# Kernel optimization log

Hardware: AMD Instinct MI355X
Metric: run time of the kernel (lower is better)

Reference implementation:

```python
import jax, jax.numpy as jnp
import numpy as np

H = 16
D_MODEL = 1024
HEAD_DIM = D_MODEL // H
NEG = -1e9


def setup_inputs() -> dict:
    key = jax.random.key(0)
    k1, k2, k3, k4, k5, k6 = jax.random.split(key, 6)
    B, L = 2, 2048
    feature = jax.random.normal(k1, (B, L, D_MODEL), dtype=jnp.float32)
    mask = jax.random.randint(k2, (B, L), 0, 2, dtype=jnp.int32)
    # Linear weights stored torch-style as [out, in]; biases zero-init per initialize().
    s = 1.0 / np.sqrt(D_MODEL)
    W_Q = jax.random.uniform(k3, (D_MODEL, D_MODEL), jnp.float32, -s, s)
    W_K = jax.random.uniform(k4, (D_MODEL, D_MODEL), jnp.float32, -s, s)
    W_V = jax.random.uniform(k5, (D_MODEL, D_MODEL), jnp.float32, -s, s)
    b_Q = jnp.zeros((D_MODEL,), jnp.float32)
    b_K = jnp.zeros((D_MODEL,), jnp.float32)
    b_V = jnp.zeros((D_MODEL,), jnp.float32)
    return {"feature": feature, "mask": mask, "W_Q": W_Q, "b_Q": b_Q,
            "W_K": W_K, "b_K": b_K, "W_V": W_V, "b_V": b_V}


def reference(feature, mask, W_Q, b_Q, W_K, b_K, W_V, b_V):
    B, L, _ = feature.shape
    scale = jnp.sqrt(jnp.float32(HEAD_DIM))
    # Projections: torch Linear is x @ W^T + b. Split into heads: [B, H, L, Dh]
    def proj(W, b):
        y = feature @ W.T + b
        return y.reshape(B, L, H, HEAD_DIM).transpose(0, 2, 1, 3)
    Q = proj(W_Q, b_Q)
    K = proj(W_K, b_K)
    V = proj(W_V, b_V)
    # Scores [B, H, Lq, Lk]
    A = jnp.einsum('bhqd,bhkd->bhqk', Q, K) / scale
    # Key-side mask broadcast over heads and query positions
    A = jnp.where(mask[:, None, None, :] == 0, jnp.float32(NEG), A)
    alpha = jax.nn.softmax(A, axis=-1)
    out = jnp.einsum('bhqk,bhkd->bhqd', alpha, V)  # [B, H, L, Dh]
    return out.transpose(0, 2, 1, 3).reshape(B, L, H * HEAD_DIM)
```

## Files before the change

### kernel.cpp

```cpp
#include <hip/hip_runtime.h>

typedef __bf16 bf16;
typedef __attribute__((ext_vector_type(4))) __bf16 bf16x4;
typedef __attribute__((ext_vector_type(8))) __bf16 bf16x8;
typedef __attribute__((ext_vector_type(4))) float f32x4;
typedef __attribute__((ext_vector_type(16))) float f32x16;
typedef unsigned int u32;

#define D_MODEL 1024
#define SEQ_L   2048
#define NHEAD   16
#define HDIM    64
#define MROWS   4096

#define S_SCALE 0.18033688f

#define FEAT_OFF  512u
#define WQ_OFF    (FEAT_OFF + 4194304u)
#define WK_OFF    (WQ_OFF + 1048576u)
#define WV_OFF    (WK_OFF + 1048576u)
#define BQ_OFF    (WV_OFF + 1048576u)
#define BK_OFF    (BQ_OFF + 1024u)
#define BV_OFF    (BK_OFF + 1024u)
#define Q_OFF     (BV_OFF + 1024u)
#define K_OFF     (Q_OFF + 4194304u)
#define V_OFF     (K_OFF + 4194304u)

typedef const __attribute__((address_space(1))) u32* gp_t;
typedef __attribute__((address_space(3))) u32* lp_t;
__device__ __forceinline__ void ld16(const bf16* g, bf16* l) {
    __builtin_amdgcn_global_load_lds((gp_t)g, (lp_t)l, 16, 0, 0);
}

__global__ void convert_in(const float* __restrict__ feat,
                           const float* __restrict__ wq, const float* __restrict__ wk,
                           const float* __restrict__ wv,
                           const float* __restrict__ bq, const float* __restrict__ bk,
                           const float* __restrict__ bv,
                           bf16* __restrict__ ws) {
    const int bid = blockIdx.x;
    const float* src; bf16* dst; int off; float sc = 1.0f;
    if (bid < 4096)      { src = feat; dst = ws + FEAT_OFF; off = bid * 1024; }
    else if (bid < 5120) { src = wq;   dst = ws + WQ_OFF;   off = (bid - 4096) * 1024; sc = S_SCALE; }
    else if (bid < 6144) { src = wk;   dst = ws + WK_OFF;   off = (bid - 5120) * 1024; }
    else if (bid < 7168) { src = wv;   dst = ws + WV_OFF;   off = (bid - 6144) * 1024; }
    else if (bid == 7168){ src = bq;   dst = ws + BQ_OFF;   off = 0; sc = S_SCALE; }
    else if (bid == 7169){ src = bk;   dst = ws + BK_OFF;   off = 0; }
    else                 { src = bv;   dst = ws + BV_OFF;   off = 0; }
    int idx = off + threadIdx.x * 4;
    float4 v = *(const float4*)(src + idx);
    bf16x4 o;
    o[0] = (bf16)(v.x * sc);
    o[1] = (bf16)(v.y * sc);
    o[2] = (bf16)(v.z * sc);
    o[3] = (bf16)(v.w * sc);
    *(bf16x4*)(dst + idx) = o;
}

__global__ __launch_bounds__(256, 2) void qkv_gemm(const bf16* __restrict__ ws,
                                                   bf16* __restrict__ wsw,
                                                   const int* __restrict__ mask) {
    __shared__ bf16 smem[3 * 128 * 64];
    bf16* Alds = smem;
    bf16* B0   = smem + 8192;
    bf16* B1   = smem + 16384;

    const int zi   = blockIdx.z;
    const int t    = threadIdx.x;
    const int lane = t & 63;
    const int wave = t >> 6;
    const int quad = lane >> 4;
    const int l16  = lane & 15;
    const int wrow = (wave >> 1) * 64;
    const int wcol = (wave & 1) * 64;
    const int r8 = lane >> 3;
    const int sl = lane & 7;
    const int sg = sl ^ r8;

    if (zi == 0) {
        const bf16* X   = ws + FEAT_OFF;
        const bf16* Wq  = ws + WQ_OFF;
        const bf16* Wk  = ws + WK_OFF;
        const int m0 = blockIdx.x * 128;
        const int n0 = blockIdx.y * 128;

        f32x4 aq[4][4], ak[4][4];
        for (int mi = 0; mi < 4; ++mi)
            for (int ni = 0; ni < 4; ++ni) {
                aq[mi][ni] = (f32x4){0.f, 0.f, 0.f, 0.f};
                ak[mi][ni] = (f32x4){0.f, 0.f, 0.f, 0.f};
            }

        for (int k0 = 0; k0 < D_MODEL; k0 += 64) {
#pragma unroll
            for (int i = 0; i < 4; ++i) {
                int ch  = wave * 4 + i;
                int row = ch * 8 + r8;
                ld16(X  + (size_t)(m0 + row) * D_MODEL + k0 + sg * 8, Alds + ch * 512);
                ld16(Wq + (size_t)(n0 + row) * D_MODEL + k0 + sg * 8, B0   + ch * 512);
                ld16(Wk + (size_t)(n0 + row) * D_MODEL + k0 + sg * 8, B1   + ch * 512);
            }
            __syncthreads();

#pragma unroll
            for (int kk = 0; kk < 2; ++kk) {
                const int sgb = quad + kk * 4;
                bf16x8 af[4];
#pragma unroll
                for (int mi = 0; mi < 4; ++mi) {
                    int row = wrow + mi * 16 + l16;
                    af[mi] = *(const bf16x8*)(&Alds[row * 64 + ((sgb ^ (row & 7)) << 3)]);
                }
                {
                    bf16x8 bfr[4];
#pragma unroll
                    for (int ni = 0; ni < 4; ++ni) {
                        int row = wcol + ni * 16 + l16;
                        bfr[ni] = *(const bf16x8*)(&B0[row * 64 + ((sgb ^ (row & 7)) << 3)]);
                    }
#pragma unroll
                    for (int mi = 0; mi < 4; ++mi)
#pragma unroll
                        for (int ni = 0; ni < 4; ++ni)
                            aq[mi][ni] = __builtin_amdgcn_mfma_f32_16x16x32_bf16(
                                af[mi], bfr[ni], aq[mi][ni], 0, 0, 0);
                }
                {
                    bf16x8 bfr[4];
#pragma unroll
                    for (int ni = 0; ni < 4; ++ni) {
                        int row = wcol + ni * 16 + l16;
                        bfr[ni] = *(const bf16x8*)(&B1[row * 64 + ((sgb ^ (row & 7)) << 3)]);
                    }
#pragma unroll
                    for (int mi = 0; mi < 4; ++mi)
#pragma unroll
                        for (int ni = 0; ni < 4; ++ni)
                            ak[mi][ni] = __builtin_amdgcn_mfma_f32_16x16x32_bf16(
                                af[mi], bfr[ni], ak[mi][ni], 0, 0, 0);
                }
            }
            __syncthreads();
        }

        bf16* Yq = wsw + Q_OFF;
        bf16* Yk = wsw + K_OFF;
        const bf16* bq = ws + BQ_OFF;
        const bf16* bk = ws + BK_OFF;
#pragma unroll
        for (int ni = 0; ni < 4; ++ni) {
            int col = n0 + wcol + ni * 16 + l16;
            float bqf = (float)bq[col];
            float bkf = (float)bk[col];
#pragma unroll
            for (int mi = 0; mi < 4; ++mi) {
                int rowb = m0 + wrow + mi * 16 + quad * 4;
#pragma unroll
                for (int r = 0; r < 4; ++r) {
                    Yq[(size_t)(rowb + r) * D_MODEL + col] = (bf16)(aq[mi][ni][r] + bqf);
                    float v = ak[mi][ni][r] + bkf;
                    if (mask[rowb + r] == 0) v = 0.f;
                    Yk[(size_t)(rowb + r) * D_MODEL + col] = (bf16)v;
                }
            }
        }
    } else {
        const bf16* Amat = ws + WV_OFF;
        const bf16* Bmat = ws + FEAT_OFF;
        const bf16* bias = ws + BV_OFF;
        bf16* Y = wsw + V_OFF;
        const int m0 = blockIdx.y * 128;
        const int n0 = blockIdx.x * 128;

        f32x4 acc[4][4];
        for (int mi = 0; mi < 4; ++mi)
            for (int ni = 0; ni < 4; ++ni)
                acc[mi][ni] = (f32x4){0.f, 0.f, 0.f, 0.f};

        for (int k0 = 0; k0 < D_MODEL; k0 += 64) {
#pragma unroll
            for (int i = 0; i < 4; ++i) {
                int ch  = wave * 4 + i;
                int row = ch * 8 + r8;
                ld16(Amat + (size_t)(m0 + row) * D_MODEL + k0 + sg * 8, Alds + ch * 512);
                ld16(Bmat + (size_t)(n0 + row) * D_MODEL + k0 + sg * 8, B0   + ch * 512);
            }
            __syncthreads();

#pragma unroll
            for (int kk = 0; kk < 2; ++kk) {
                const int sgb = quad + kk * 4;
                bf16x8 af[4], bfr[4];
#pragma unroll
                for (int mi = 0; mi < 4; ++mi) {
                    int row = wrow + mi * 16 + l16;
                    af[mi] = *(const bf16x8*)(&Alds[row * 64 + ((sgb ^ (row & 7)) << 3)]);
                }
#pragma unroll
                for (int ni = 0; ni < 4; ++ni) {
                    int row = wcol + ni * 16 + l16;
                    bfr[ni] = *(const bf16x8*)(&B0[row * 64 + ((sgb ^ (row & 7)) << 3)]);
                }
#pragma unroll
                for (int mi = 0; mi < 4; ++mi)
#pragma unroll
                    for (int ni = 0; ni < 4; ++ni)
                        acc[mi][ni] = __builtin_amdgcn_mfma_f32_16x16x32_bf16(
                            af[mi], bfr[ni], acc[mi][ni], 0, 0, 0);
            }
            __syncthreads();
        }

#pragma unroll
        for (int mi = 0; mi < 4; ++mi) {
#pragma unroll
            for (int r = 0; r < 4; ++r) {
                int rowv = m0 + wrow + mi * 16 + quad * 4 + r;
                float bvf = (float)bias[rowv];
#pragma unroll
                for (int ni = 0; ni < 4; ++ni) {
                    int col = n0 + wcol + ni * 16 + l16;
                    float v = acc[mi][ni][r] + bvf;
                    if (mask[col] == 0) v = 0.f;
                    size_t addr = (size_t)(col >> 11) * 2097152u +
                                  (size_t)rowv * 2048u + (col & 2047);
                    Y[addr] = (bf16)v;
                }
            }
        }
    }
}

__global__ __launch_bounds__(256, 4) void attn_kernel(
    const bf16* __restrict__ ws,
    const int* __restrict__ mask, float* __restrict__ out) {
    const int bh  = blockIdx.x;
    const int qt  = blockIdx.y;
    const int b   = bh >> 4, h = bh & 15;
    const int t    = threadIdx.x;
    const int lane = t & 63;
    const int wave = t >> 6;
    const int half = lane >> 5;
    const int l31  = lane & 31;

    __shared__ bf16 Klds[2][64 * 64];
    __shared__ bf16 Vlds[2][64 * 64];

    const bf16* Qh  = ws + Q_OFF + (size_t)(b * SEQ_L) * D_MODEL + h * HDIM;
    const bf16* Kh  = ws + K_OFF + (size_t)(b * SEQ_L) * D_MODEL + h * HDIM;
    const bf16* Vth = ws + V_OFF + (size_t)b * 2097152u + (size_t)(h * HDIM) * SEQ_L;

    const int qrow0 = qt * 128 + wave * 32;
    bf16x8 qf[4];
#pragma unroll
    for (int ks = 0; ks < 4; ++ks)
        qf[ks] = *(const bf16x8*)(Qh + (size_t)(qrow0 + l31) * D_MODEL
                                  + ks * 16 + half * 8);

    bf16x8 ones;
#pragma unroll
    for (int j = 0; j < 8; ++j) ones[j] = (bf16)1.0f;

    f32x16 o[2], lacc;
    int nm = 0;
#pragma unroll
    for (int i = 0; i < 16; ++i) { o[0][i] = 0.f; o[1][i] = 0.f; lacc[i] = 0.f; }

    const int srow = (lane >> 3);
    const int sg   = (lane & 7) ^ srow;

#define STAGE(bb, kt)                                                          \
    do {                                                                       \
        _Pragma("unroll")                                                      \
        for (int i = 0; i < 2; ++i) {                                          \
            int row = i * 32 + wave * 8 + srow;                                \
            ld16(Kh + (size_t)((kt) + row) * D_MODEL + sg * 8,                 \
                 &Klds[bb][i * 2048 + wave * 512]);                            \
            ld16(Vth + (size_t)row * SEQ_L + (kt) + sg * 8,                    \
                 &Vlds[bb][i * 2048 + wave * 512]);                            \
        }                                                                      \
    } while (0)

    STAGE(0, 0);
    __syncthreads();

    int cur = 0;
    for (int kt = 0; kt < SEQ_L; kt += 64) {
        if (kt + 64 < SEQ_L) STAGE(cur ^ 1, kt + 64);

        int mv = mask[b * SEQ_L + kt + lane];
        nm += (int)__popcll(__ballot(mv != 0));

        f32x16 st[2];
#pragma unroll
        for (int ktile = 0; ktile < 2; ++ktile) {
#pragma unroll
            for (int i = 0; i < 16; ++i) st[ktile][i] = 0.f;
#pragma unroll
            for (int ks = 0; ks < 4; ++ks) {
                const int row  = ktile * 32 + l31;
                const int slot = (ks * 2 + half) ^ (l31 & 7);
                bf16x8 kf = *(const bf16x8*)(&Klds[cur][row * 64 + slot * 8]);
                st[ktile] = __builtin_amdgcn_mfma_f32_32x32x16_bf16(
                    kf, qf[ks], st[ktile], 0, 0, 0);
            }
        }

        bf16x4 pk[2][4];
#pragma unroll
        for (int ktile = 0; ktile < 2; ++ktile) {
#pragma unroll
            for (int g = 0; g < 4; ++g) {
                bf16x4 pkv;
#pragma unroll
                for (int j = 0; j < 4; ++j)
                    pkv[j] = (bf16)__builtin_amdgcn_exp2f(st[ktile][g * 4 + j]);
                pk[ktile][g] = pkv;
            }
        }

        bf16x8 pf[4];
#pragma unroll
        for (int ks = 0; ks < 4; ++ks) {
            const int k1 = ks & 1, kt2 = ks >> 1;
            uint2 a  = __builtin_bit_cast(uint2, pk[kt2][2 * k1]);
            uint2 bb = __builtin_bit_cast(uint2, pk[kt2][2 * k1 + 1]);
            uint2 keep, send;
            keep.x = half ? bb.x : a.x;  keep.y = half ? bb.y : a.y;
            send.x = half ? a.x : bb.x;  send.y = half ? a.y : bb.y;
            uint2 recv;
            recv.x = (unsigned)__shfl_xor((int)send.x, 32);
            recv.y = (unsigned)__shfl_xor((int)send.y, 32);
            uint4 frag;
            frag.x = half ? recv.x : keep.x;
            frag.y = half ? recv.y : keep.y;
            frag.z = half ? keep.x : recv.x;
            frag.w = half ? keep.y : recv.y;
            pf[ks] = __builtin_bit_cast(bf16x8, frag);
        }

#pragma unroll
        for (int ks = 0; ks < 4; ++ks)
            lacc = __builtin_amdgcn_mfma_f32_32x32x16_bf16(pf[ks], ones, lacc, 0, 0, 0);
#pragma unroll
        for (int dt = 0; dt < 2; ++dt) {
#pragma unroll
            for (int ks = 0; ks < 4; ++ks) {
                const int row  = dt * 32 + l31;
                const int slot = (ks * 2 + half) ^ (l31 & 7);
                bf16x8 vf = *(const bf16x8*)(&Vlds[cur][row * 64 + slot * 8]);
                o[dt] = __builtin_amdgcn_mfma_f32_32x32x16_bf16(
                    pf[ks], vf, o[dt], 0, 0, 0);
            }
        }

        __syncthreads();
        cur ^= 1;
    }
#undef STAGE

    const float corr = (float)(SEQ_L - nm);
#pragma unroll
    for (int r = 0; r < 16; ++r) {
        const int q32 = (r & 3) + 8 * (r >> 2) + 4 * half;
        const int q = qrow0 + q32;
        const size_t base = ((size_t)(b * SEQ_L + q)) * D_MODEL + h * HDIM;
        const float rl = 1.0f / fmaxf(lacc[r] - corr, 1e-30f);
        out[base + l31]      = o[0][r] * rl;
        out[base + 32 + l31] = o[1][r] * rl;
    }
}

extern "C" void kernel_launch(void* const* d_in, const int* in_sizes, int n_in,
                              void* d_out, int out_size, void* d_ws, size_t ws_size,
                              hipStream_t stream) {
    const float* feat = (const float*)d_in[0];
    const int*   mask = (const int*)d_in[1];
    const float* Wq = (const float*)d_in[2];
    const float* bq = (const float*)d_in[3];
    const float* Wk = (const float*)d_in[4];
    const float* bk = (const float*)d_in[5];
    const float* Wv = (const float*)d_in[6];
    const float* bv = (const float*)d_in[7];

    bf16* ws = (bf16*)d_ws;

    convert_in<<<7171, 256, 0, stream>>>(feat, Wq, Wk, Wv, bq, bk, bv, ws);

    dim3 g1(32, 8, 2);
    qkv_gemm<<<g1, 256, 0, stream>>>(ws, ws, mask);

    dim3 g2(2 * NHEAD, SEQ_L / 128);
    attn_kernel<<<g2, 256, 0, stream>>>(ws, mask, (float*)d_out);
}
```

Before: 171.6 us.

## Split key range across two wave groups per block and merge via LDS

Doubles the attention block to 512 threads, with two groups of four waves each processing half of the key sequence for the same query rows. Partial outputs and row sums from the second group are written to shared memory and added by the first group before normalization. This is meant to raise parallelism and shorten the serial key loop per block. In exchange it doubles LDS use per block and adds a final reduction step.

```diff
diff --git a/kernel.cpp b/kernel.cpp
--- a/kernel.cpp
+++ b/kernel.cpp
@@ -231,7 +231,7 @@
     }
 }
 
-__global__ __launch_bounds__(256, 4) void attn_kernel(
+__global__ __launch_bounds__(512, 4) void attn_kernel(
     const bf16* __restrict__ ws,
     const int* __restrict__ mask, float* __restrict__ out) {
     const int bh  = blockIdx.x;
@@ -240,17 +240,21 @@
     const int t    = threadIdx.x;
     const int lane = t & 63;
     const int wave = t >> 6;
+    const int qh   = wave & 3;
+    const int kh   = wave >> 2;
     const int half = lane >> 5;
     const int l31  = lane & 31;
-
-    __shared__ bf16 Klds[2][64 * 64];
-    __shared__ bf16 Vlds[2][64 * 64];
+    const int kt0  = kh * 1024;
+
+    __shared__ bf16 smem[32768];
+    bf16* Kb = smem;
+    bf16* Vb = smem + 16384;
 
     const bf16* Qh  = ws + Q_OFF + (size_t)(b * SEQ_L) * D_MODEL + h * HDIM;
     const bf16* Kh  = ws + K_OFF + (size_t)(b * SEQ_L) * D_MODEL + h * HDIM;
     const bf16* Vth = ws + V_OFF + (size_t)b * 2097152u + (size_t)(h * HDIM) * SEQ_L;
 
-    const int qrow0 = qt * 128 + wave * 32;
+    const int qrow0 = qt * 128 + qh * 32;
     bf16x8 qf[4];
 #pragma unroll
     for (int ks = 0; ks < 4; ++ks)
@@ -273,24 +277,26 @@
     do {                                                                       \
         _Pragma("unroll")                                                      \
         for (int i = 0; i < 2; ++i) {                                          \
-            int row = i * 32 + wave * 8 + srow;                                \
+            int row = i * 32 + qh * 8 + srow;                                  \
             ld16(Kh + (size_t)((kt) + row) * D_MODEL + sg * 8,                 \
-                 &Klds[bb][i * 2048 + wave * 512]);                            \
+                 Kb + (kh * 2 + (bb)) * 4096 + i * 2048 + qh * 512);           \
             ld16(Vth + (size_t)row * SEQ_L + (kt) + sg * 8,                    \
-                 &Vlds[bb][i * 2048 + wave * 512]);                            \
+                 Vb + (kh * 2 + (bb)) * 4096 + i * 2048 + qh * 512);           \
         }                                                                      \
     } while (0)
 
-    STAGE(0, 0);
+    STAGE(0, kt0);
     __syncthreads();
 
     int cur = 0;
-    for (int kt = 0; kt < SEQ_L; kt += 64) {
-        if (kt + 64 < SEQ_L) STAGE(cur ^ 1, kt + 64);
+    for (int it = 0; it < 16; ++it) {
+        const int kt = kt0 + it * 64;
+        if (it < 15) STAGE(cur ^ 1, kt + 64);
 
         int mv = mask[b * SEQ_L + kt + lane];
         nm += (int)__popcll(__ballot(mv != 0));
 
+        const bf16* Kcur = Kb + (kh * 2 + cur) * 4096;
         f32x16 st[2];
 #pragma unroll
         for (int ktile = 0; ktile < 2; ++ktile) {
@@ -300,7 +306,7 @@
             for (int ks = 0; ks < 4; ++ks) {
                 const int row  = ktile * 32 + l31;
                 const int slot = (ks * 2 + half) ^ (l31 & 7);
-                bf16x8 kf = *(const bf16x8*)(&Klds[cur][row * 64 + slot * 8]);
+                bf16x8 kf = *(const bf16x8*)(&Kcur[row * 64 + slot * 8]);
                 st[ktile] = __builtin_amdgcn_mfma_f32_32x32x16_bf16(
                     kf, qf[ks], st[ktile], 0, 0, 0);
             }
@@ -339,6 +345,7 @@
             pf[ks] = __builtin_bit_cast(bf16x8, frag);
         }
 
+        const bf16* Vcur = Vb + (kh * 2 + cur) * 4096;
 #pragma unroll
         for (int ks = 0; ks < 4; ++ks)
             lacc = __builtin_amdgcn_mfma_f32_32x32x16_bf16(pf[ks], ones, lacc, 0, 0, 0);
@@ -348,7 +355,7 @@
             for (int ks = 0; ks < 4; ++ks) {
                 const int row  = dt * 32 + l31;
                 const int slot = (ks * 2 + half) ^ (l31 & 7);
-                bf16x8 vf = *(const bf16x8*)(&Vlds[cur][row * 64 + slot * 8]);
+                bf16x8 vf = *(const bf16x8*)(&Vcur[row * 64 + slot * 8]);
                 o[dt] = __builtin_amdgcn_mfma_f32_32x32x16_bf16(
                     pf[ks], vf, o[dt], 0, 0, 0);
             }
@@ -359,15 +366,29 @@
     }
 #undef STAGE
 
-    const float corr = (float)(SEQ_L - nm);
-#pragma unroll
-    for (int r = 0; r < 16; ++r) {
-        const int q32 = (r & 3) + 8 * (r >> 2) + 4 * half;
-        const int q = qrow0 + q32;
-        const size_t base = ((size_t)(b * SEQ_L + q)) * D_MODEL + h * HDIM;
-        const float rl = 1.0f / fmaxf(lacc[r] - corr, 1e-30f);
-        out[base + l31]      = o[0][r] * rl;
-        out[base + 32 + l31] = o[1][r] * rl;
+    const float corr = (float)(1024 - nm);
+    float* ex = (float*)smem;
+    const int slot = qh * 64 + lane;
+    if (kh == 1) {
+#pragma unroll
+        for (int r = 0; r < 16; ++r) {
+            ex[r * 256 + slot]        = o[0][r];
+            ex[(16 + r) * 256 + slot] = o[1][r];
+            ex[(32 + r) * 256 + slot] = lacc[r] - corr;
+        }
+    }
+    __syncthreads();
+    if (kh == 0) {
+#pragma unroll
+        for (int r = 0; r < 16; ++r) {
+            const int q32 = (r & 3) + 8 * (r >> 2) + 4 * half;
+            const int q = qrow0 + q32;
+            const size_t base = ((size_t)(b * SEQ_L + q)) * D_MODEL + h * HDIM;
+            const float l  = (lacc[r] - corr) + ex[(32 + r) * 256 + slot];
+            const float rl = 1.0f / fmaxf(l, 1e-30f);
+            out[base + l31]      = (o[0][r] + ex[r * 256 + slot]) * rl;
+            out[base + 32 + l31] = (o[1][r] + ex[(16 + r) * 256 + slot]) * rl;
+        }
     }
 }
 
@@ -391,5 +412,5 @@
     qkv_gemm<<<g1, 256, 0, stream>>>(ws, ws, mask);
 
     dim3 g2(2 * NHEAD, SEQ_L / 128);
-    attn_kernel<<<g2, 256, 0, stream>>>(ws, mask, (float*)d_out);
+    attn_kernel<<<g2, 512, 0, stream>>>(ws, mask, (float*)d_out);
 }
```

After: 161.2 us. 6.1% less time.
